# Performance work log

Measured on AMD Instinct MI355X. Metric: run time of the kernel, lower is better.

The kernel has to match this reference:

```python
import jax, jax.numpy as jnp
import numpy as np

T, N = 24, 2048
INPUT_DIM, HIDDEN, MEDIATE, SOCIAL, OUT_DIM = 2, 64, 128, 64, 2
N_SIZE = 2
CELL = 0.3
T_OBS, T_PRED = 9, 19
WIN = (N_SIZE + 1) ** 2  # (N_size+1)^2 = 9 window cells


def _social_pool(h, coords, mask):
    """Faithful social pooling for N_size=2, grid_cell_size=0.3.

    torch builds a dynamic grid, scatter-adds every agent's h into its cell,
    then gathers grid[int(x-R):int(x+R), int(y-R):int(y+R)] per agent.
    With R=0.3 and integer positions >= 4 (guaranteed by the margin), that
    slice is exactly the single cell (x-1, y-1), broadcast over the 3x3
    window. We compute it as a pairwise match without materializing a grid.
    Runs under torch.no_grad() -> stop_gradient.
    """
    margin = 2 * N_SIZE * CELL
    lt = jnp.stack([coords[:, 0].min(), coords[:, 1].min()]) - margin
    p = jnp.floor((coords - lt) / CELL).astype(jnp.int32)            # [N,2]
    p = p * mask.astype(jnp.int32)[:, None]                          # masked agents -> cell (0,0)
    q = p - 1                                                        # gathered cell per agent
    match = (p[None, :, 0] == q[:, None, 0]) & (p[None, :, 1] == q[:, None, 1])  # [i,j]
    cell_val = match.astype(h.dtype) @ h                             # [N,hidden] scatter-add + gather
    Hf = jnp.tile(cell_val, (1, WIN)) * mask[:, None]                # broadcast over 3x3 window, flat
    return jax.lax.stop_gradient(Hf)


def _forward(X, part_masks, all_h_t, all_c_t, Y, W_in, b_in, W_soc, b_soc,
             W_ih, W_hh, b_ih, b_hh, W_out, b_out, T_obs, T_pred):
    relu = jax.nn.relu  # dropout_prob = 0 -> Phi == ReLU

    def lstm(z, h, c):
        g = z @ W_ih.T + b_ih + h @ W_hh.T + b_hh
        i, f, gg, o = jnp.split(g, 4, axis=1)
        c = jax.nn.sigmoid(f) * c + jax.nn.sigmoid(i) * jnp.tanh(gg)
        h = jax.nn.sigmoid(o) * jnp.tanh(c)
        return h, c

    def cell_out(r, h, c, coords, m):
        Hf = _social_pool(h, coords, m)
        e = relu(Hf @ W_soc.T + b_soc)
        z = jnp.concatenate([r, e], axis=1)
        h, c = lstm(z, h, c)
        out = (h @ W_out.T + b_out) * m[:, None]
        return h, c, out

    def step_obs(carry, inp):
        h, c = carry
        x, m = inp
        r = relu(x @ W_in.T + b_in)
        h, c, out = cell_out(r, h, c, x, m)
        return (h, c), out

    (h, c), outs_obs = jax.lax.scan(
        step_obs, (all_h_t, all_c_t), (X[:T_obs + 1], part_masks[:T_obs + 1]))

    def step_pred(carry, inp):
        h, c, last_pt, prev_out = carry
        x, m = inp
        r = relu(last_pt @ W_in.T + b_in)
        h, c, out = cell_out(r, h, c, x, m)
        # torch: last_point = outputs[frame_idx - 1] AFTER the frame runs
        return (h, c, prev_out, out), out

    carry0 = (h, c, X[T_obs + 1], outs_obs[-1])
    _, outs_pred = jax.lax.scan(
        step_pred, carry0, (X[T_obs + 1:T_pred + 1], part_masks[T_obs + 1:T_pred + 1]))

    tail = jnp.zeros((X.shape[0] - T_pred - 1, X.shape[1], OUT_DIM), X.dtype)
    return jnp.concatenate([outs_obs, outs_pred, tail], axis=0)


def setup_inputs() -> dict:
    key = jax.random.key(0)
    ks = jax.random.split(key, 13)

    def lin(kw, kb, out_d, in_d):  # torch nn.Linear default init
        lim = 1.0 / float(np.sqrt(in_d))
        W = jax.random.uniform(kw, (out_d, in_d), minval=-lim, maxval=lim, dtype=jnp.float32)
        b = jax.random.uniform(kb, (out_d,), minval=-lim, maxval=lim, dtype=jnp.float32)
        return W, b

    W_in, b_in = lin(ks[0], ks[1], MEDIATE, INPUT_DIM)
    W_soc, b_soc = lin(ks[2], ks[3], SOCIAL, WIN * HIDDEN)
    W_ih, b_ih = lin(ks[4], ks[5], 4 * HIDDEN, MEDIATE + SOCIAL)
    W_hh, b_hh = lin(ks[6], ks[7], 4 * HIDDEN, HIDDEN)
    W_out, b_out = lin(ks[8], ks[9], OUT_DIM, HIDDEN)

    X = jax.random.normal(ks[10], (T, N, INPUT_DIM), dtype=jnp.float32) * 10.0  # meter-scale coords
    part_masks = (jax.random.uniform(ks[11], (T, N)) < 0.9).astype(jnp.float32)  # binary presence mask
    Y = jax.random.normal(ks[12], (T, N, INPUT_DIM), dtype=jnp.float32)  # unused by forward
    all_h_t = jnp.zeros((N, HIDDEN), jnp.float32)
    all_c_t = jnp.zeros((N, HIDDEN), jnp.float32)

    return {"X": X, "part_masks": part_masks, "all_h_t": all_h_t, "all_c_t": all_c_t,
            "Y": Y, "T_obs": T_OBS, "T_pred": T_PRED,
            "W_in": W_in, "b_in": b_in, "W_soc": W_soc, "b_soc": b_soc,
            "W_ih": W_ih, "W_hh": W_hh, "b_ih": b_ih, "b_hh": b_hh,
            "W_out": W_out, "b_out": b_out}


def reference(X, part_masks, all_h_t, all_c_t, Y, T_obs, T_pred,
              W_in, b_in, W_soc, b_soc, W_ih, W_hh, b_ih, b_hh, W_out, b_out):
    return _forward(X, part_masks, all_h_t, all_c_t, Y, W_in, b_in, W_soc, b_soc,
                    W_ih, W_hh, b_ih, b_hh, W_out, b_out, int(T_obs), int(T_pred))
```

## Files before the change

### kernel.cpp

```cpp
#include <hip/hip_runtime.h>
#include <math.h>


#define N_AG   2048
#define STEPS  20
#define CAP    12
#define NSRV   21
#define MAGIC  0x13572468

typedef short short8 __attribute__((ext_vector_type(8)));
typedef float f32x4  __attribute__((ext_vector_type(4)));
union FU { uint4 q; short8 v; };

__device__ __forceinline__ void pack8(const float* v, uint4& hq, uint4& lq) {
    unsigned uh[4], ul[4];
    #pragma unroll
    for (int w = 0; w < 4; w++) {
        float v0 = v[2 * w], v1 = v[2 * w + 1];
        unsigned h;
        asm("v_cvt_pk_bf16_f32 %0, %1, %2" : "=v"(h) : "v"(v0), "v"(v1));
        float f0 = __uint_as_float(h << 16);
        float f1 = __uint_as_float(h & 0xffff0000u);
        float r0 = v0 - f0, r1 = v1 - f1;
        unsigned l;
        asm("v_cvt_pk_bf16_f32 %0, %1, %2" : "=v"(l) : "v"(r0), "v"(r1));
        uh[w] = h; ul[w] = l;
    }
    hq = make_uint4(uh[0], uh[1], uh[2], uh[3]);
    lq = make_uint4(ul[0], ul[1], ul[2], ul[3]);
}

__device__ __forceinline__ int khash(int k) {
    return (int)(((unsigned)k * 2654435761u) >> 21);
}

__device__ __forceinline__ float fsigm(float x) {
    return __builtin_amdgcn_rcpf(1.f + __expf(-x));
}
__device__ __forceinline__ float ftanh(float x) {
    float e = __expf(2.f * x);
    return 1.f - 2.f * __builtin_amdgcn_rcpf(e + 1.f);
}

__device__ __forceinline__ void bar_lds() {
    asm volatile("s_waitcnt lgkmcnt(0)\n\ts_barrier" ::: "memory");
}

__device__ __forceinline__ void ast(int* p_, int v) {
    __hip_atomic_store(p_, v, __ATOMIC_RELAXED, __HIP_MEMORY_SCOPE_AGENT);
}
__device__ __forceinline__ void astf(float* p_, float v) {
    __hip_atomic_store(p_, v, __ATOMIC_RELAXED, __HIP_MEMORY_SCOPE_AGENT);
}
__device__ __forceinline__ unsigned long long aldu64(const unsigned long long* p_) {
    return __hip_atomic_load(p_, __ATOMIC_RELAXED, __HIP_MEMORY_SCOPE_AGENT);
}

__device__ __forceinline__ void edot_frag(
    int m5, int s5, float a0, float a1,
    float (*cvs)[68], const float* sWefP, const float* sBsoc,
    uint4* zshq, uint4* zslq)
{
    cvs[m5][s5] = a0; cvs[m5][s5 + 32] = a1;
    float acc0 = sBsoc[s5],       acc1 = sBsoc[s5 + 32];
    float acc0b = 0.f,            acc1b = 0.f;
    const float* w0p = &sWefP[s5 * 65];
    const float* w1p = &sWefP[(s5 + 32) * 65];
    const float4* cw = (const float4*)&cvs[m5][0];
    #pragma unroll
    for (int k4 = 0; k4 < 16; k4 += 2) {
        float4 ca = cw[k4];
        float4 cb = cw[k4 + 1];
        int k = k4 * 4;
        acc0  += ca.x * w0p[k]     + ca.y * w0p[k + 1] + ca.z * w0p[k + 2] + ca.w * w0p[k + 3];
        acc1  += ca.x * w1p[k]     + ca.y * w1p[k + 1] + ca.z * w1p[k + 2] + ca.w * w1p[k + 3];
        acc0b += cb.x * w0p[k + 4] + cb.y * w0p[k + 5] + cb.z * w0p[k + 6] + cb.w * w0p[k + 7];
        acc1b += cb.x * w1p[k + 4] + cb.y * w1p[k + 5] + cb.z * w1p[k + 6] + cb.w * w1p[k + 7];
    }
    acc0 = fmaxf(acc0 + acc0b, 0.f);
    acc1 = fmaxf(acc1 + acc1b, 0.f);
    const int base = (m5 & 1) * 32;
    float v[8];
    #pragma unroll
    for (int jj = 0; jj < 8; jj++) {
        int c = s5 * 8 + jj;
        int srcl = base + ((c < 32 ? c : c - 32) & 31);
        float va = __shfl(acc0, srcl, 64);
        float vb = __shfl(acc1, srcl, 64);
        v[jj] = (c < 32) ? va : vb;
    }
    if (s5 < 8)
        pack8(v, zshq[(16 + s5) * 17 + m5], zslq[(16 + s5) * 17 + m5]);
}

struct KP {
    const float *X, *masks, *h_in, *c_in;
    const float *Win, *bin, *Wsoc, *bsoc, *Wih, *Whh, *bih, *bhh, *Wout, *bout;
    float *Wef;
    int *mcnt, *midx, *need, *flags;
    float *out;
    unsigned long long *hist;
};

__global__ __launch_bounds__(512, 1) void k_all(KP p)
{
    __shared__ __align__(16) uint4 zshq[544];
    __shared__ __align__(16) uint4 zslq[544];
    __shared__ float gbuf[16][258];
    __shared__ __align__(16) float cvs[16][68];
    __shared__ __align__(16) float hs[16][68];
    __shared__ float sWefP[64 * 65];
    __shared__ float2 sWinP[16 * 17];
    __shared__ float sBinP[16 * 9];
    __shared__ float sX[11][16][2];
    __shared__ float sMask[STEPS][16];
    __shared__ int   sCnt[STEPS][16];
    __shared__ int   sNeed[19][16];
    __shared__ int   sMidx[STEPS][16][CAP];
    __shared__ float sBsoc[64], sBc[256], sWout[128], sBout[2];
    __shared__ uint4 sE0h[8], sE0l[8];
    __shared__ int kk[N_AG];
    __shared__ int head[N_AG];
    __shared__ int nxt[N_AG];
    __shared__ float red[512];

    const int tid = threadIdx.x;
    const int bxg = blockIdx.x;

    if (bxg < NSRV) {
        const int sb = bxg;
        {
            int lo = sb * 780;
            int hi = (sb == NSRV - 1) ? 16384 : lo + 780;
            for (int i = lo + tid; i < hi; i += 512)
                p.out[20 * N_AG * 2 + i] = 0.f;
        }
        if (sb == 20) {
            for (int i = tid; i < 4096; i += 512) {
                int s = i >> 6, k = i & 63;
                float a = 0.f;
                #pragma unroll
                for (int w = 0; w < 9; w++) a += p.Wsoc[s * 576 + w * 64 + k];
                astf(&p.Wef[i], a);
            }
            __syncthreads();
            if (tid == 0) ast(&p.flags[20], MAGIC);
            return;
        }

        const int t = sb;
        const float* Xt = p.X + t * N_AG * 2;

        float mnx = 1e30f, mny = 1e30f;
        for (int i = tid; i < N_AG; i += 512) {
            mnx = fminf(mnx, Xt[2 * i]);
            mny = fminf(mny, Xt[2 * i + 1]);
        }
        red[tid] = mnx; __syncthreads();
        for (int s = 256; s > 0; s >>= 1) { if (tid < s) red[tid] = fminf(red[tid], red[tid + s]); __syncthreads(); }
        float ltx = red[0]; __syncthreads();
        red[tid] = mny; __syncthreads();
        for (int s = 256; s > 0; s >>= 1) { if (tid < s) red[tid] = fminf(red[tid], red[tid + s]); __syncthreads(); }
        float lty = red[0]; __syncthreads();
        ltx -= 1.2f;
        lty -= 1.2f;

        for (int i = tid; i < N_AG; i += 512) {
            float m = p.masks[t * N_AG + i];
            int px = (int)floorf((Xt[2 * i]     - ltx) / 0.3f);
            int py = (int)floorf((Xt[2 * i + 1] - lty) / 0.3f);
            int im = (int)m;
            px *= im; py *= im;
            kk[i] = px * 65536 + py;
            head[i] = -1;
            if (t >= 1) ast(&p.need[(t - 1) * N_AG + i], 0);
        }
        __syncthreads();
        for (int j = tid; j < N_AG; j += 512) {
            int kj = kk[j];
            if (kj != 0) nxt[j] = atomicExch(&head[khash(kj)], j);
        }
        __syncthreads();
        for (int i = tid; i < N_AG; i += 512) {
            int ki = kk[i];
            int cnt = 0;
            int base = (t * N_AG + i) * CAP;
            if (ki != 0) {
                int tkey = ki - 65537;
                int lst[CAP];
                for (int j = head[khash(tkey)]; j >= 0; j = nxt[j]) {
                    if (kk[j] == tkey) { if (cnt < CAP) lst[cnt] = j; cnt++; }
                }
                if (cnt > CAP) cnt = CAP;
                for (int a = 1; a < cnt; a++) {
                    int v = lst[a]; int b = a - 1;
                    while (b >= 0 && lst[b] > v) { lst[b + 1] = lst[b]; b--; }
                    lst[b + 1] = v;
                }
                for (int a = 0; a < cnt; a++) {
                    ast(&p.midx[base + a], lst[a]);
                    if (t >= 1) ast(&p.need[(t - 1) * N_AG + lst[a]], 1);
                }
            }
            ast(&p.mcnt[t * N_AG + i], cnt);
        }
        __syncthreads();
        if (tid == 0) ast(&p.flags[t], MAGIC);
        return;
    }

    const int bx    = bxg - NSRV;
    const int wbase = bx * 16;
    const int wv    = tid >> 6, lane = tid & 63;
    const int mA    = lane & 15, quad = lane >> 4;
    const int nt0   = 2 * wv;
    const int m0w   = wv, m1w = wv + 8;
    const int m5    = tid >> 5, s5 = tid & 31;

    if (tid < 256) sBc[tid] = p.bih[tid] + p.bhh[tid];
    if (tid < 128) {
        sWout[tid] = p.Wout[tid];
        int c = tid;
        sWinP[(c >> 3) * 17 + (c & 7)] = make_float2(p.Win[2 * c], p.Win[2 * c + 1]);
        sBinP[(c >> 3) * 9 + (c & 7)] = p.bin[c];
    }
    if (tid < 64) sBsoc[tid] = p.bsoc[tid];
    if (tid < 2)  sBout[tid] = p.bout[tid];
    if (tid < 8) {
        float v[8];
        #pragma unroll
        for (int j = 0; j < 8; j++) v[j] = fmaxf(p.bsoc[tid * 8 + j], 0.f);
        pack8(v, sE0h[tid], sE0l[tid]);
    }
    if (tid < 352) { int tt = tid / 32, r = tid % 32;
                     sX[tt][r >> 1][r & 1] = p.X[tt * (N_AG * 2) + (wbase + (r >> 1)) * 2 + (r & 1)]; }
    if (tid < 320) { int tt = tid / 16, m2 = tid % 16;
                     sMask[tt][m2] = p.masks[tt * N_AG + wbase + m2]; }

    float c0, c1;
    {
        hs[m0w][lane] = p.h_in[(wbase + m0w) * 64 + lane];
        hs[m1w][lane] = p.h_in[(wbase + m1w) * 64 + lane];
        c0 = p.c_in[(wbase + m0w) * 64 + lane];
        c1 = p.c_in[(wbase + m1w) * 64 + lane];
    }

    FU wh[2][8], wl[2][8];
    #pragma unroll
    for (int e = 0; e < 2; e++) {
        int g = (nt0 + e) * 16 + mA;
        #pragma unroll
        for (int kt = 0; kt < 8; kt++) {
            int k0 = kt * 32 + quad * 8;
            const float* src = (k0 < 192) ? (p.Wih + g * 192 + k0)
                                          : (p.Whh + g * 64 + (k0 - 192));
            float v[8];
            #pragma unroll
            for (int j = 0; j < 8; j++) v[j] = src[j];
            pack8(v, wh[e][kt].q, wl[e][kt].q);
        }
    }

    if (tid < NSRV) {
        while (__hip_atomic_load(&p.flags[tid], __ATOMIC_RELAXED,
                                 __HIP_MEMORY_SCOPE_AGENT) != MAGIC) { }
    }
    __syncthreads();

    if (tid < 320) { int tt = tid / 16, m2 = tid % 16;
                     sCnt[tt][m2] = p.mcnt[tt * N_AG + wbase + m2]; }
    if (tid < 304) { int s = tid / 16, m2 = tid % 16;
                     sNeed[s][m2] = p.need[s * N_AG + wbase + m2]; }
    for (int i = tid; i < 4096; i += 512) sWefP[(i >> 6) * 65 + (i & 63)] = p.Wef[i];
    for (int i = tid; i < STEPS * 16 * CAP; i += 512) {
        int tt = i / (16 * CAP), r = i % (16 * CAP), m2 = r / CAP, n = r % CAP;
        sMidx[tt][m2][n] = p.midx[(tt * N_AG + wbase + m2) * CAP + n];
    }
    __syncthreads();

    {
        if (lane < 32) {
            int a = lane & 1, s5r = lane >> 1;
            int m = a ? m1w : m0w;
            float px = sX[0][m][0], py = sX[0][m][1];
            float v[8];
            #pragma unroll
            for (int j = 0; j < 8; j++) {
                float2 w2 = sWinP[s5r * 17 + j];
                v[j] = fmaxf(w2.x * px + w2.y * py + sBinP[s5r * 9 + j], 0.f);
            }
            pack8(v, zshq[s5r * 17 + m], zslq[s5r * 17 + m]);
        } else if (lane < 48) {
            int idx = lane - 32, a = idx & 1, s58 = idx >> 1;
            int m = a ? m1w : m0w;
            float v[8];
            #pragma unroll
            for (int j = 0; j < 8; j++) v[j] = hs[m][s58 * 8 + j];
            pack8(v, zshq[(24 + s58) * 17 + m], zslq[(24 + s58) * 17 + m]);
        } else {
            int idx = lane - 48, a = idx & 1, s58 = idx >> 1;
            int m = a ? m1w : m0w;
            if (sCnt[0][m] == 0) {
                zshq[(16 + s58) * 17 + m] = sE0h[s58];
                zslq[(16 + s58) * 17 + m] = sE0l[s58];
            }
        }
        int cnt0 = sCnt[0][m5];
        if (cnt0 > 0) {
            float a0 = 0.f, a1 = 0.f;
            for (int n = 0; n < cnt0; n++) {
                int r = sMidx[0][m5][n];
                a0 += p.h_in[r * 64 + s5];
                a1 += p.h_in[r * 64 + s5 + 32];
            }
            edot_frag(m5, s5, a0, a1, cvs, sWefP, sBsoc, zshq, zslq);
        }
    }
    bar_lds();

    float op0x = 0.f, op0y = 0.f, op1x = 0.f, op1y = 0.f;

    #pragma unroll 1
    for (int t = 0; t < STEPS; t++) {
        f32x4 a0v = {0.f, 0.f, 0.f, 0.f};
        f32x4 a1v = {0.f, 0.f, 0.f, 0.f};
        #pragma unroll
        for (int kt = 0; kt < 8; kt++) {
            int fi = (kt * 4 + quad) * 17 + mA;
            FU az, bz;
            az.q = zshq[fi];
            bz.q = zslq[fi];
            a0v = __builtin_amdgcn_mfma_f32_16x16x32_bf16(az.v, wh[0][kt].v, a0v, 0, 0, 0);
            a1v = __builtin_amdgcn_mfma_f32_16x16x32_bf16(az.v, wh[1][kt].v, a1v, 0, 0, 0);
            a0v = __builtin_amdgcn_mfma_f32_16x16x32_bf16(bz.v, wh[0][kt].v, a0v, 0, 0, 0);
            a1v = __builtin_amdgcn_mfma_f32_16x16x32_bf16(bz.v, wh[1][kt].v, a1v, 0, 0, 0);
            a0v = __builtin_amdgcn_mfma_f32_16x16x32_bf16(az.v, wl[0][kt].v, a0v, 0, 0, 0);
            a1v = __builtin_amdgcn_mfma_f32_16x16x32_bf16(az.v, wl[1][kt].v, a1v, 0, 0, 0);
        }
        #pragma unroll
        for (int r = 0; r < 4; r++) {
            int row = quad * 4 + r;
            gbuf[row][nt0 * 16 + mA]       = a0v[r];
            gbuf[row][(nt0 + 1) * 16 + mA] = a1v[r];
        }
        bar_lds();

        {
            const int hid = lane;
            float hn0, hn1;
            {
                float gi = gbuf[m0w][hid]       + sBc[hid];
                float gf = gbuf[m0w][64 + hid]  + sBc[64 + hid];
                float gR = gbuf[m0w][128 + hid] + sBc[128 + hid];
                float go = gbuf[m0w][192 + hid] + sBc[192 + hid];
                float cn = fsigm(gf) * c0 + fsigm(gi) * ftanh(gR);
                hn0 = fsigm(go) * ftanh(cn);
                c0 = cn;
                hs[m0w][hid] = hn0;
            }
            {
                float gi = gbuf[m1w][hid]       + sBc[hid];
                float gf = gbuf[m1w][64 + hid]  + sBc[64 + hid];
                float gR = gbuf[m1w][128 + hid] + sBc[128 + hid];
                float go = gbuf[m1w][192 + hid] + sBc[192 + hid];
                float cn = fsigm(gf) * c1 + fsigm(gi) * ftanh(gR);
                hn1 = fsigm(go) * ftanh(cn);
                c1 = cn;
                hs[m1w][hid] = hn1;
            }
            if (t <= 18) {
                unsigned long long* hp = p.hist + (size_t)t * (N_AG * 64);
                unsigned long long tg = ((unsigned long long)(t + 1)) << 32;
                if (sNeed[t][m0w])
                    __hip_atomic_store(&hp[(wbase + m0w) * 64 + hid],
                                       tg | (unsigned long long)__float_as_uint(hn0),
                                       __ATOMIC_RELAXED, __HIP_MEMORY_SCOPE_AGENT);
                if (sNeed[t][m1w])
                    __hip_atomic_store(&hp[(wbase + m1w) * 64 + hid],
                                       tg | (unsigned long long)__float_as_uint(hn1),
                                       __ATOMIC_RELAXED, __HIP_MEMORY_SCOPE_AGENT);
            }

            const unsigned long long* hb = p.hist + (size_t)t * (N_AG * 64);
            int cntN = 0, rfirst = -1, rsecond = -1;
            unsigned long long pw0 = 0, pw1 = 0, qw0 = 0, qw1 = 0;
            if (t < STEPS - 1) {
                cntN = sCnt[t + 1][m5];
                if (cntN > 0) {
                    rfirst = sMidx[t + 1][m5][0];
                    pw0 = aldu64(&hb[rfirst * 64 + s5]);
                    pw1 = aldu64(&hb[rfirst * 64 + s5 + 32]);
                    if (cntN > 1) {
                        rsecond = sMidx[t + 1][m5][1];
                        qw0 = aldu64(&hb[rsecond * 64 + s5]);
                        qw1 = aldu64(&hb[rsecond * 64 + s5 + 32]);
                    }
                }
            }

            float w0 = sWout[hid], w1 = sWout[64 + hid];
            float p00 = hn0 * w0, p01 = hn0 * w1;
            float p10 = hn1 * w0, p11 = hn1 * w1;
            #pragma unroll
            for (int off = 32; off >= 1; off >>= 1) {
                p00 += __shfl_xor(p00, off);
                p01 += __shfl_xor(p01, off);
                p10 += __shfl_xor(p10, off);
                p11 += __shfl_xor(p11, off);
            }
            float mk0 = sMask[t][m0w], mk1 = sMask[t][m1w];
            float o00 = (p00 + sBout[0]) * mk0, o01 = (p01 + sBout[1]) * mk0;
            float o10 = (p10 + sBout[0]) * mk1, o11 = (p11 + sBout[1]) * mk1;
            if (lane == 0)
                *(float2*)&p.out[(t * N_AG + wbase + m0w) * 2] = make_float2(o00, o01);
            if (lane == 1)
                *(float2*)&p.out[(t * N_AG + wbase + m1w) * 2] = make_float2(o10, o11);

            if (t < STEPS - 1) {
                const int tn = t + 1;
                if (lane < 32) {
                    int a = lane & 1, s5r = lane >> 1;
                    int m = a ? m1w : m0w;
                    float px, py;
                    if (tn <= 10) { px = sX[tn][m][0]; py = sX[tn][m][1]; }
                    else          { px = a ? op1x : op0x;
                                    py = a ? op1y : op0y; }
                    float v[8];
                    #pragma unroll
                    for (int j = 0; j < 8; j++) {
                        float2 w2 = sWinP[s5r * 17 + j];
                        v[j] = fmaxf(w2.x * px + w2.y * py + sBinP[s5r * 9 + j], 0.f);
                    }
                    pack8(v, zshq[s5r * 17 + m], zslq[s5r * 17 + m]);
                } else if (lane < 48) {
                    int idx = lane - 32, a = idx & 1, s58 = idx >> 1;
                    int m = a ? m1w : m0w;
                    const float4* hr = (const float4*)&hs[m][s58 * 8];
                    float4 h0 = hr[0], h1 = hr[1];
                    float v[8] = { h0.x, h0.y, h0.z, h0.w, h1.x, h1.y, h1.z, h1.w };
                    pack8(v, zshq[(24 + s58) * 17 + m], zslq[(24 + s58) * 17 + m]);
                } else {
                    int idx = lane - 48, a = idx & 1, s58 = idx >> 1;
                    int m = a ? m1w : m0w;
                    if (sCnt[tn][m] == 0) {
                        zshq[(16 + s58) * 17 + m] = sE0h[s58];
                        zslq[(16 + s58) * 17 + m] = sE0l[s58];
                    }
                }
            }

            if (cntN > 0) {
                const unsigned tagw = (unsigned)(t + 1);
                while ((unsigned)(pw0 >> 32) != tagw || (unsigned)(pw1 >> 32) != tagw) {
                    pw0 = aldu64(&hb[rfirst * 64 + s5]);
                    pw1 = aldu64(&hb[rfirst * 64 + s5 + 32]);
                }
                float a0 = __uint_as_float((unsigned)pw0);
                float a1 = __uint_as_float((unsigned)pw1);
                if (cntN > 1) {
                    while ((unsigned)(qw0 >> 32) != tagw || (unsigned)(qw1 >> 32) != tagw) {
                        qw0 = aldu64(&hb[rsecond * 64 + s5]);
                        qw1 = aldu64(&hb[rsecond * 64 + s5 + 32]);
                    }
                    a0 += __uint_as_float((unsigned)qw0);
                    a1 += __uint_as_float((unsigned)qw1);
                    for (int n = 2; n < cntN; n++) {
                        int r = sMidx[t + 1][m5][n];
                        unsigned long long w0_, w1_;
                        do {
                            w0_ = aldu64(&hb[r * 64 + s5]);
                            w1_ = aldu64(&hb[r * 64 + s5 + 32]);
                        } while ((unsigned)(w0_ >> 32) != tagw || (unsigned)(w1_ >> 32) != tagw);
                        a0 += __uint_as_float((unsigned)w0_);
                        a1 += __uint_as_float((unsigned)w1_);
                    }
                }
                edot_frag(m5, s5, a0, a1, cvs, sWefP, sBsoc, zshq, zslq);
            }

            op0x = o00; op0y = o01;
            op1x = o10; op1y = o11;
        }
        bar_lds();
    }
}

extern "C" void kernel_launch(void* const* d_in, const int* in_sizes, int n_in,
                              void* d_out, int out_size, void* d_ws, size_t ws_size,
                              hipStream_t stream)
{
    KP kp;
    kp.X     = (const float*)d_in[0];
    kp.masks = (const float*)d_in[1];
    kp.h_in  = (const float*)d_in[2];
    kp.c_in  = (const float*)d_in[3];
    kp.Win   = (const float*)d_in[7];
    kp.bin   = (const float*)d_in[8];
    kp.Wsoc  = (const float*)d_in[9];
    kp.bsoc  = (const float*)d_in[10];
    kp.Wih   = (const float*)d_in[11];
    kp.Whh   = (const float*)d_in[12];
    kp.bih   = (const float*)d_in[13];
    kp.bhh   = (const float*)d_in[14];
    kp.Wout  = (const float*)d_in[15];
    kp.bout  = (const float*)d_in[16];
    kp.out   = (float*)d_out;

    unsigned long long* hist = (unsigned long long*)d_ws;
    float* Wef  = (float*)(hist + 19 * N_AG * 64);
    int*   need = (int*)(Wef + 4096);
    int*   mcnt = need + 19 * N_AG;
    int*   midx = mcnt + STEPS * N_AG;
    int*   flags = midx + STEPS * N_AG * CAP;

    kp.hist = hist; kp.Wef = Wef; kp.need = need; kp.mcnt = mcnt;
    kp.midx = midx; kp.flags = flags;

    k_all<<<NSRV + 128, 512, 0, stream>>>(kp);
}
```

Measured before the change: 178.6 us.

## Fold output projection into next step's gate MFMA and widen Wef LDS reads

Wave 0 now computes the output projection of the previous step's hidden state with extra bf16-split MFMAs over the hidden-state slice of the packed input tile (k-tiles 6 and 7). It writes the two logits into spare gbuf columns, so output t-1 and the fed-back coordinates are read from LDS instead of a per-step 6-round shuffle reduction. The shuffle path is kept only for the final step. Separately, the social-embedding weight buffer is repadded to a 66-float stride so the dot product can use float2 LDS loads. The intent is to shorten the serial per-step critical path. The cost is extra MFMA work and register pressure on wave 0, plus a possible change in LDS bank-conflict behaviour.

New measurement: 169.7 us. 4.9% less time.

```diff
diff --git a/kernel.cpp b/kernel.cpp
--- a/kernel.cpp
+++ b/kernel.cpp
@@ -64,18 +64,18 @@
     cvs[m5][s5] = a0; cvs[m5][s5 + 32] = a1;
     float acc0 = sBsoc[s5],       acc1 = sBsoc[s5 + 32];
     float acc0b = 0.f,            acc1b = 0.f;
-    const float* w0p = &sWefP[s5 * 65];
-    const float* w1p = &sWefP[(s5 + 32) * 65];
+    const float2* w0q = (const float2*)&sWefP[s5 * 66];
+    const float2* w1q = (const float2*)&sWefP[(s5 + 32) * 66];
     const float4* cw = (const float4*)&cvs[m5][0];
     #pragma unroll
-    for (int k4 = 0; k4 < 16; k4 += 2) {
+    for (int k4 = 0; k4 < 16; k4++) {
         float4 ca = cw[k4];
-        float4 cb = cw[k4 + 1];
-        int k = k4 * 4;
-        acc0  += ca.x * w0p[k]     + ca.y * w0p[k + 1] + ca.z * w0p[k + 2] + ca.w * w0p[k + 3];
-        acc1  += ca.x * w1p[k]     + ca.y * w1p[k + 1] + ca.z * w1p[k + 2] + ca.w * w1p[k + 3];
-        acc0b += cb.x * w0p[k + 4] + cb.y * w0p[k + 5] + cb.z * w0p[k + 6] + cb.w * w0p[k + 7];
-        acc1b += cb.x * w1p[k + 4] + cb.y * w1p[k + 5] + cb.z * w1p[k + 6] + cb.w * w1p[k + 7];
+        float2 wa0 = w0q[2 * k4], wb0 = w0q[2 * k4 + 1];
+        float2 wa1 = w1q[2 * k4], wb1 = w1q[2 * k4 + 1];
+        acc0  += ca.x * wa0.x + ca.y * wa0.y;
+        acc0b += ca.z * wb0.x + ca.w * wb0.y;
+        acc1  += ca.x * wa1.x + ca.y * wa1.y;
+        acc1b += ca.z * wb1.x + ca.w * wb1.y;
     }
     acc0 = fmaxf(acc0 + acc0b, 0.f);
     acc1 = fmaxf(acc1 + acc1b, 0.f);
@@ -106,10 +106,10 @@
 {
     __shared__ __align__(16) uint4 zshq[544];
     __shared__ __align__(16) uint4 zslq[544];
-    __shared__ float gbuf[16][258];
+    __shared__ float gbuf[16][260];
     __shared__ __align__(16) float cvs[16][68];
     __shared__ __align__(16) float hs[16][68];
-    __shared__ float sWefP[64 * 65];
+    __shared__ __align__(16) float sWefP[64 * 66];
     __shared__ float2 sWinP[16 * 17];
     __shared__ float sBinP[16 * 9];
     __shared__ float sX[11][16][2];
@@ -260,6 +260,18 @@
             pack8(v, wh[e][kt].q, wl[e][kt].q);
         }
     }
+    FU woh[2], wol[2];
+    #pragma unroll
+    for (int e2 = 0; e2 < 2; e2++) {
+        int kt = 6 + e2;
+        float v[8];
+        #pragma unroll
+        for (int j = 0; j < 8; j++) {
+            int k0 = kt * 32 + quad * 8 + j - 192;
+            v[j] = (mA < 2) ? p.Wout[mA * 64 + k0] : 0.f;
+        }
+        pack8(v, woh[e2].q, wol[e2].q);
+    }
 
     if (tid < NSRV) {
         while (__hip_atomic_load(&p.flags[tid], __ATOMIC_RELAXED,
@@ -271,7 +283,7 @@
                      sCnt[tt][m2] = p.mcnt[tt * N_AG + wbase + m2]; }
     if (tid < 304) { int s = tid / 16, m2 = tid % 16;
                      sNeed[s][m2] = p.need[s * N_AG + wbase + m2]; }
-    for (int i = tid; i < 4096; i += 512) sWefP[(i >> 6) * 65 + (i & 63)] = p.Wef[i];
+    for (int i = tid; i < 4096; i += 512) sWefP[(i >> 6) * 66 + (i & 63)] = p.Wef[i];
     for (int i = tid; i < STEPS * 16 * CAP; i += 512) {
         int tt = i / (16 * CAP), r = i % (16 * CAP), m2 = r / CAP, n = r % CAP;
         sMidx[tt][m2][n] = p.midx[(tt * N_AG + wbase + m2) * CAP + n];
@@ -318,12 +330,11 @@
     }
     bar_lds();
 
-    float op0x = 0.f, op0y = 0.f, op1x = 0.f, op1y = 0.f;
-
     #pragma unroll 1
     for (int t = 0; t < STEPS; t++) {
         f32x4 a0v = {0.f, 0.f, 0.f, 0.f};
         f32x4 a1v = {0.f, 0.f, 0.f, 0.f};
+        f32x4 ovv = {0.f, 0.f, 0.f, 0.f};
         #pragma unroll
         for (int kt = 0; kt < 8; kt++) {
             int fi = (kt * 4 + quad) * 17 + mA;
@@ -336,12 +347,23 @@
             a1v = __builtin_amdgcn_mfma_f32_16x16x32_bf16(bz.v, wh[1][kt].v, a1v, 0, 0, 0);
             a0v = __builtin_amdgcn_mfma_f32_16x16x32_bf16(az.v, wl[0][kt].v, a0v, 0, 0, 0);
             a1v = __builtin_amdgcn_mfma_f32_16x16x32_bf16(az.v, wl[1][kt].v, a1v, 0, 0, 0);
+            if (kt >= 6 && wv == 0) {
+                int e2 = kt - 6;
+                ovv = __builtin_amdgcn_mfma_f32_16x16x32_bf16(az.v, woh[e2].v, ovv, 0, 0, 0);
+                ovv = __builtin_amdgcn_mfma_f32_16x16x32_bf16(bz.v, woh[e2].v, ovv, 0, 0, 0);
+                ovv = __builtin_amdgcn_mfma_f32_16x16x32_bf16(az.v, wol[e2].v, ovv, 0, 0, 0);
+            }
         }
         #pragma unroll
         for (int r = 0; r < 4; r++) {
             int row = quad * 4 + r;
             gbuf[row][nt0 * 16 + mA]       = a0v[r];
             gbuf[row][(nt0 + 1) * 16 + mA] = a1v[r];
+        }
+        if (wv == 0 && mA < 2) {
+            #pragma unroll
+            for (int r = 0; r < 4; r++)
+                gbuf[quad * 4 + r][256 + mA] = ovv[r];
         }
         bar_lds();
 
@@ -398,23 +420,37 @@
                 }
             }
 
-            float w0 = sWout[hid], w1 = sWout[64 + hid];
-            float p00 = hn0 * w0, p01 = hn0 * w1;
-            float p10 = hn1 * w0, p11 = hn1 * w1;
-            #pragma unroll
-            for (int off = 32; off >= 1; off >>= 1) {
-                p00 += __shfl_xor(p00, off);
-                p01 += __shfl_xor(p01, off);
-                p10 += __shfl_xor(p10, off);
-                p11 += __shfl_xor(p11, off);
-            }
-            float mk0 = sMask[t][m0w], mk1 = sMask[t][m1w];
-            float o00 = (p00 + sBout[0]) * mk0, o01 = (p01 + sBout[1]) * mk0;
-            float o10 = (p10 + sBout[0]) * mk1, o11 = (p11 + sBout[1]) * mk1;
-            if (lane == 0)
-                *(float2*)&p.out[(t * N_AG + wbase + m0w) * 2] = make_float2(o00, o01);
-            if (lane == 1)
-                *(float2*)&p.out[(t * N_AG + wbase + m1w) * 2] = make_float2(o10, o11);
+            float q00 = 0.f, q01 = 0.f, q10 = 0.f, q11 = 0.f;
+            if (t >= 1) {
+                float mk0p = sMask[t - 1][m0w], mk1p = sMask[t - 1][m1w];
+                q00 = (gbuf[m0w][256] + sBout[0]) * mk0p;
+                q01 = (gbuf[m0w][257] + sBout[1]) * mk0p;
+                q10 = (gbuf[m1w][256] + sBout[0]) * mk1p;
+                q11 = (gbuf[m1w][257] + sBout[1]) * mk1p;
+                if (lane == 0)
+                    *(float2*)&p.out[((t - 1) * N_AG + wbase + m0w) * 2] = make_float2(q00, q01);
+                if (lane == 1)
+                    *(float2*)&p.out[((t - 1) * N_AG + wbase + m1w) * 2] = make_float2(q10, q11);
+            }
+            if (t == STEPS - 1) {
+                float w0 = sWout[hid], w1 = sWout[64 + hid];
+                float p00 = hn0 * w0, p01 = hn0 * w1;
+                float p10 = hn1 * w0, p11 = hn1 * w1;
+                #pragma unroll
+                for (int off = 32; off >= 1; off >>= 1) {
+                    p00 += __shfl_xor(p00, off);
+                    p01 += __shfl_xor(p01, off);
+                    p10 += __shfl_xor(p10, off);
+                    p11 += __shfl_xor(p11, off);
+                }
+                float mk0 = sMask[t][m0w], mk1 = sMask[t][m1w];
+                if (lane == 0)
+                    *(float2*)&p.out[(t * N_AG + wbase + m0w) * 2] =
+                        make_float2((p00 + sBout[0]) * mk0, (p01 + sBout[1]) * mk0);
+                if (lane == 1)
+                    *(float2*)&p.out[(t * N_AG + wbase + m1w) * 2] =
+                        make_float2((p10 + sBout[0]) * mk1, (p11 + sBout[1]) * mk1);
+            }
 
             if (t < STEPS - 1) {
                 const int tn = t + 1;
@@ -423,8 +459,8 @@
                     int m = a ? m1w : m0w;
                     float px, py;
                     if (tn <= 10) { px = sX[tn][m][0]; py = sX[tn][m][1]; }
-                    else          { px = a ? op1x : op0x;
-                                    py = a ? op1y : op0y; }
+                    else          { px = a ? q10 : q00;
+                                    py = a ? q11 : q01; }
                     float v[8];
                     #pragma unroll
                     for (int j = 0; j < 8; j++) {
@@ -477,9 +513,6 @@
                 }
                 edot_frag(m5, s5, a0, a1, cvs, sWefP, sBsoc, zshq, zslq);
             }
-
-            op0x = o00; op0y = o01;
-            op1x = o10; op1y = o11;
         }
         bar_lds();
     }
```
